# Optimization experiments

Hardware: AMD Instinct MI355X
Metric: run time of the kernel (lower is better)

## Reference

```python
import jax, jax.numpy as jnp
import numpy as np

N = 16384          # number of input points
K = 16             # kNN neighbors for EdgeConv
SCALES = (4096, 1024, 256)
DIM = 256
EC_HID = 64        # EdgeConv output dim
MLP_HID = 128


def _sqdist(a, b):
    # squared euclidean distance matrix: (Na, Nb)
    return (jnp.sum(a * a, axis=1, keepdims=True)
            - 2.0 * (a @ b.T)
            + jnp.sum(b * b, axis=1)[None, :])


def _fps(points, n):
    # farthest point sampling, deterministic start at index 0
    d = jnp.sum((points - points[0]) ** 2, axis=1)  # (N,)

    def step(d, _):
        nxt = jnp.argmax(d)
        d = jnp.minimum(d, jnp.sum((points - points[nxt]) ** 2, axis=1))
        return d, nxt

    _, rest = jax.lax.scan(step, d, None, length=n - 1)
    return jnp.concatenate([jnp.zeros((1,), dtype=rest.dtype), rest])


def setup_inputs() -> dict:
    key = jax.random.key(0)
    ks = jax.random.split(key, 10)

    def lin(k, fi, fo):
        return (jax.random.normal(k, (fi, fo), jnp.float32) / np.sqrt(fi)).astype(jnp.float32)

    nsc = len(SCALES)
    return {
        "points": jax.random.normal(ks[0], (N, 3), jnp.float32),
        # EdgeConv MLP: Linear(6,64) -> ReLU -> Linear(64,64)
        "ew1": lin(ks[1], 6, EC_HID), "eb1": jnp.zeros((EC_HID,), jnp.float32),
        "ew2": lin(ks[2], EC_HID, EC_HID), "eb2": jnp.zeros((EC_HID,), jnp.float32),
        # per-scale MLPs: Linear(64,128) -> ReLU -> Linear(128,256), stacked over scales
        "mw1": jnp.stack([lin(jax.random.fold_in(ks[3], i), EC_HID, MLP_HID) for i in range(nsc)]),
        "mb1": jnp.zeros((nsc, MLP_HID), jnp.float32),
        "mw2": jnp.stack([lin(jax.random.fold_in(ks[4], i), MLP_HID, DIM) for i in range(nsc)]),
        "mb2": jnp.zeros((nsc, DIM), jnp.float32),
    }


def _edge_conv(points, ew1, eb1, ew2, eb2):
    # kNN graph (loop=False): exclude self via +inf diagonal; indices not differentiated
    d = jax.lax.stop_gradient(_sqdist(points, points))
    d = d.at[jnp.arange(N), jnp.arange(N)].set(jnp.inf)
    _, idx = jax.lax.top_k(-d, K)                      # (N, K) neighbor indices
    x_i = points[:, None, :]                           # (N, 1, 3) centers
    x_j = points[idx]                                  # (N, K, 3) neighbors
    ef = jnp.concatenate([jnp.broadcast_to(x_i, (N, K, 3)), x_j - x_i], axis=-1)  # (N,K,6)
    h = jax.nn.relu(ef @ ew1 + eb1) @ ew2 + eb2        # (N, K, 64)
    # scatter_max over centers == max over the K neighbor axis (every center has K edges)
    return jnp.max(h, axis=1)                          # (N, 64)


def reference(points, ew1, eb1, ew2, eb2, mw1, mb1, mw2, mb2):
    feats = _edge_conv(points, ew1, eb1, ew2, eb2)     # (N, 64)
    outs = []
    prev_pts = None
    for i, scale in enumerate(SCALES):
        if i == 0:
            fi = _fps(points, scale)
            sp = points[fi]
            sf = feats[fi]
        else:
            fi = _fps(prev_pts, scale)
            sp = prev_pts[fi]
            nn = jnp.argmin(_sqdist(sp, points), axis=1)  # nearest source point per query
            sf = feats[nn]
        lf = jax.nn.relu(sf @ mw1[i] + mb1[i]) @ mw2[i] + mb2[i]  # (scale, DIM)
        outs.append(sp)
        outs.append(lf)
        prev_pts = sp
    return tuple(outs)
```

## Files before the change

kernel.cpp:

```cpp
#include <hip/hip_runtime.h>
#include <cfloat>
#include <cstdint>

#define N_PTS 16384
#define KNN_K 16
#define KNN_TILE 512
#define CERT_EPS 3e-6f

struct FpsSmem {
    float sx[N_PTS];
    unsigned long long slots[2][16];
    int cw2[2][2];
    int cand_idx[64];
    int cand_cnt;
    int more_flag;
    double red_d[16];
};

template <int CTRL>
__device__ __forceinline__ unsigned dpp_mov_u32(unsigned v) {
    return (unsigned)__builtin_amdgcn_update_dpp((int)v, (int)v, CTRL, 0xF, 0xF, false);
}

__device__ __forceinline__ void cross_slot_reduce(unsigned long long k, float& M1, int& G1) {
    unsigned hi = (unsigned)(k >> 32), lo = (unsigned)k;
#define RSTEP(CTRL)                                          \
    {                                                        \
        const unsigned ohi = dpp_mov_u32<CTRL>(hi);          \
        const unsigned olo = dpp_mov_u32<CTRL>(lo);          \
        const bool b = (ohi > hi) || (ohi == hi && olo > lo);\
        hi = b ? ohi : hi;                                   \
        lo = b ? olo : lo;                                   \
    }
    RSTEP(0x121)
    RSTEP(0x122)
    RSTEP(0x124)
    RSTEP(0x128)
#undef RSTEP
    M1 = __uint_as_float(hi);
    G1 = (int)(~lo);
}

template <int P, bool IND>
__device__ __forceinline__ void fps_body(FpsSmem& sm, const float* __restrict__ pts,
                                         const int* __restrict__ idx,
                                         int n_out, int* __restrict__ fi) {
    constexpr int T = 1024;
    constexpr int NW = T / 64;
    const int tid = threadIdx.x;
    const int wave = tid >> 6, lane = tid & 63;

    __syncthreads();

    if (tid < 32) sm.slots[tid >> 4][tid & 15] = 0ull;
    if (tid < 4) sm.cw2[tid >> 1][tid & 1] = 0;

    float yr[P], zr[P], c[P];
    const int g0 = IND ? idx[0] : 0;
    const float sx0 = pts[g0 * 3 + 0], sy0 = pts[g0 * 3 + 1], sz0 = pts[g0 * 3 + 2];
    if (tid == 0) fi[0] = g0;

    float m1 = -1.0f, m2 = -1.0f;
    int g1 = 0x7fffffff;
#pragma unroll
    for (int q = 0; q < P; ++q) {
        const int g = tid + q * T;
        const int gg = IND ? idx[g] : g;
        const float x = pts[gg * 3 + 0];
        const float y = pts[gg * 3 + 1];
        const float z = pts[gg * 3 + 2];
        sm.sx[g] = x;
        yr[q] = y;
        zr[q] = z;
        const float dx = x - sx0, dy = y - sy0, dz = z - sz0;
        const float t = fmaf(dx, dx, fmaf(dy, dy, dz * dz));
        const float nc = fminf(FLT_MAX, t);
        c[q] = nc;
        const bool gt = nc > m1;
        m2 = fmaxf(m2, fminf(nc, m1));
        m1 = fmaxf(m1, nc);
        g1 = gt ? g : g1;
    }
    __syncthreads();
    {
        const unsigned long long key =
            ((unsigned long long)__float_as_uint(m1) << 32) |
            (unsigned long long)(~(unsigned)g1);
        atomicMax(&sm.slots[1][tid & 15], key);
    }

    for (int s = 1; s < n_out; ++s) {
        __syncthreads();
        const int par = s & 1;

        const unsigned long long k0 = sm.slots[par][lane & 15];
        float M1;
        int G1;
        cross_slot_reduce(k0, M1, G1);
        const float thr = M1 - M1 * CERT_EPS;

        int wg = G1;
        if (IND) wg = idx[G1];
        float nx = sm.sx[G1];
        float ny = pts[wg * 3 + 1];
        float nz = pts[wg * 3 + 2];

        if (tid < 16) sm.slots[par ^ 1][tid] = 0ull;
        if (tid == 0) { sm.cw2[par ^ 1][0] = 0; sm.cw2[par ^ 1][1] = 0; }

        const unsigned long long bal = __ballot(m1 >= thr);
        if (lane == 0) atomicAdd(&sm.cw2[par][0], (int)__popcll(bal));
        if (g1 == G1) sm.cw2[par][1] = (m2 >= thr) ? 1 : 0;

        __syncthreads();
        const int2 tw = *reinterpret_cast<const int2*>(&sm.cw2[par][0]);
        const int total = tw.x, wfl = tw.y;

        if (total > 1 || wfl) {
            unsigned miss = 0;
#pragma unroll
            for (int q = 0; q < P; ++q)
                if (c[q] >= thr) miss |= (1u << q);
            double BD = -1.0;
            int BG = 0x7fffffff;
            for (;;) {
                if (tid == 0) { sm.cand_cnt = 0; sm.more_flag = 0; }
                __syncthreads();
#pragma unroll
                for (int q = 0; q < P; ++q) {
                    if (miss & (1u << q)) {
                        int slot = atomicAdd(&sm.cand_cnt, 1);
                        if (slot < 64) {
                            sm.cand_idx[slot] = tid + q * T;
                            miss &= ~(1u << q);
                        } else {
                            sm.more_flag = 1;
                        }
                    }
                }
                __syncthreads();
                int ncand = sm.cand_cnt;
                if (ncand > 64) ncand = 64;
                for (int ci = 0; ci < ncand; ++ci) {
                    const int g = sm.cand_idx[ci];
                    const int gg = IND ? idx[g] : g;
                    const double qx = (double)pts[gg * 3 + 0];
                    const double qy = (double)pts[gg * 3 + 1];
                    const double qz = (double)pts[gg * 3 + 2];
                    double dmin = DBL_MAX;
                    for (int i = tid; i < s; i += T) {
                        const int h = fi[i];
                        double ddx = qx - (double)pts[h * 3 + 0];
                        double ddy = qy - (double)pts[h * 3 + 1];
                        double ddz = qz - (double)pts[h * 3 + 2];
                        double dd = ddx * ddx + ddy * ddy + ddz * ddz;
                        dmin = (dd < dmin) ? dd : dmin;
                    }
                    for (int off = 32; off; off >>= 1) {
                        double od = __shfl_xor(dmin, off);
                        dmin = (od < dmin) ? od : dmin;
                    }
                    if (lane == 0) sm.red_d[wave] = dmin;
                    __syncthreads();
                    double dall = sm.red_d[0];
#pragma unroll
                    for (int w = 1; w < NW; ++w) dall = (sm.red_d[w] < dall) ? sm.red_d[w] : dall;
                    if (dall > BD || (dall == BD && g < BG)) { BD = dall; BG = g; }
                    __syncthreads();
                }
                int mf = sm.more_flag;
                __syncthreads();
                if (!mf) break;
            }
            G1 = BG;
            wg = IND ? idx[G1] : G1;
            nx = pts[wg * 3 + 0];
            ny = pts[wg * 3 + 1];
            nz = pts[wg * 3 + 2];
        }

        if (tid == 0) fi[s] = wg;
        if (s == n_out - 1) break;

        float nm1 = -1.0f, nm2 = -1.0f;
        int ng1 = 0x7fffffff;
#pragma unroll
        for (int q = 0; q < P; ++q) {
            const float dx = sm.sx[tid + q * T] - nx;
            const float dy = yr[q] - ny, dz = zr[q] - nz;
            const float t = fmaf(dx, dx, fmaf(dy, dy, dz * dz));
            const float nc = fminf(c[q], t);
            c[q] = nc;
            const bool gt = nc > nm1;
            nm2 = fmaxf(nm2, fminf(nc, nm1));
            nm1 = fmaxf(nm1, nc);
            ng1 = gt ? (tid + q * T) : ng1;
        }
        m1 = nm1; m2 = nm2; g1 = ng1;
        const unsigned long long key =
            ((unsigned long long)__float_as_uint(m1) << 32) |
            (unsigned long long)(~(unsigned)g1);
        atomicMax(&sm.slots[par ^ 1][tid & 15], key);
    }
}

struct KnnSmem {
    float sx[KNN_TILE], sy[KNN_TILE], sz[KNN_TILE];
    float w1[6 * 64], b1v[64], w2[64 * 64], b2v[64];
};

__device__ __forceinline__ void knn_edge_body(
    KnnSmem& sm, const float* __restrict__ pts,
    const float* __restrict__ ew1, const float* __restrict__ eb1,
    const float* __restrict__ ew2, const float* __restrict__ eb2,
    float* __restrict__ feats, int qb) {
    for (int t = threadIdx.x; t < 6 * 64; t += 1024) sm.w1[t] = ew1[t];
    for (int t = threadIdx.x; t < 64; t += 1024) { sm.b1v[t] = eb1[t]; sm.b2v[t] = eb2[t]; }
    for (int t = threadIdx.x; t < 64 * 64; t += 1024) sm.w2[t] = ew2[t];

    const int wave = threadIdx.x >> 6;
    const int lane = threadIdx.x & 63;
    const int qi = qb * 16 + wave;
    const double qxd = (double)pts[qi * 3 + 0];
    const double qyd = (double)pts[qi * 3 + 1];
    const double qzd = (double)pts[qi * 3 + 2];

    double ld[16];
    int li[16];
#pragma unroll
    for (int s = 0; s < 16; ++s) { ld[s] = DBL_MAX; li[s] = 0x7fffffff; }
    double md = DBL_MAX; int mj = 0x7fffffff; int mslot = 0;

    for (int t0 = 0; t0 < N_PTS; t0 += KNN_TILE) {
        __syncthreads();
        for (int t = threadIdx.x; t < KNN_TILE; t += 1024) {
            sm.sx[t] = pts[(t0 + t) * 3 + 0];
            sm.sy[t] = pts[(t0 + t) * 3 + 1];
            sm.sz[t] = pts[(t0 + t) * 3 + 2];
        }
        __syncthreads();
#pragma unroll
        for (int m = 0; m < KNN_TILE / 64; ++m) {
            const int cc = lane + m * 64;
            const int j = t0 + cc;
            if (j == qi) continue;
            double dx = qxd - (double)sm.sx[cc];
            double dy = qyd - (double)sm.sy[cc];
            double dz = qzd - (double)sm.sz[cc];
            double dd = dx * dx + dy * dy + dz * dz;
            if (dd < md || (dd == md && j < mj)) {
#pragma unroll
                for (int s = 0; s < 16; ++s)
                    if (s == mslot) { ld[s] = dd; li[s] = j; }
                md = -1.0; mj = -1; mslot = 0;
#pragma unroll
                for (int s = 0; s < 16; ++s) {
                    bool g = (ld[s] > md) || (ld[s] == md && li[s] > mj);
                    if (g) { md = ld[s]; mj = li[s]; mslot = s; }
                }
            }
        }
    }

    const float xi = pts[qi * 3], yi = pts[qi * 3 + 1], zi = pts[qi * 3 + 2];
    float acc = -FLT_MAX;
    for (int r = 0; r < KNN_K; ++r) {
        double cd = DBL_MAX; int cj = 0x7fffffff; int cs = 0;
#pragma unroll
        for (int s = 0; s < 16; ++s) {
            bool l = (ld[s] < cd) || (ld[s] == cd && li[s] < cj);
            if (l) { cd = ld[s]; cj = li[s]; cs = s; }
        }
        double wd = cd; int wj = cj;
        for (int off = 32; off; off >>= 1) {
            double od = __shfl_xor(wd, off);
            int oj = __shfl_xor(wj, off);
            if (od < wd || (od == wd && oj < wj)) { wd = od; wj = oj; }
        }
        if (cd == wd && cj == wj) {
#pragma unroll
            for (int s = 0; s < 16; ++s)
                if (s == cs) { ld[s] = DBL_MAX; li[s] = 0x7fffffff; }
        }
        const float xj = pts[wj * 3], yj = pts[wj * 3 + 1], zj = pts[wj * 3 + 2];
        const float f3 = xj - xi, f4 = yj - yi, f5 = zj - zi;
        float h1 = sm.b1v[lane];
        h1 = fmaf(xi, sm.w1[0 * 64 + lane], h1);
        h1 = fmaf(yi, sm.w1[1 * 64 + lane], h1);
        h1 = fmaf(zi, sm.w1[2 * 64 + lane], h1);
        h1 = fmaf(f3, sm.w1[3 * 64 + lane], h1);
        h1 = fmaf(f4, sm.w1[4 * 64 + lane], h1);
        h1 = fmaf(f5, sm.w1[5 * 64 + lane], h1);
        h1 = fmaxf(h1, 0.0f);
        float h2 = sm.b2v[lane];
        for (int d = 0; d < 64; ++d)
            h2 = fmaf(__shfl(h1, d), sm.w2[d * 64 + lane], h2);
        acc = fmaxf(acc, h2);
    }
    feats[qi * 64 + lane] = acc;
}

__global__ __launch_bounds__(1024)
void mega_kernel(const float* __restrict__ pts,
                 const float* __restrict__ ew1, const float* __restrict__ eb1,
                 const float* __restrict__ ew2, const float* __restrict__ eb2,
                 float* __restrict__ feats,
                 int* __restrict__ fi0, int* __restrict__ fi1, int* __restrict__ fi2,
                 float* __restrict__ sp0, float* __restrict__ sp1,
                 float* __restrict__ sp2) {
    constexpr size_t SMEM_BYTES =
        sizeof(FpsSmem) > sizeof(KnnSmem) ? sizeof(FpsSmem) : sizeof(KnnSmem);
    __shared__ __align__(16) char raw[SMEM_BYTES];
    if (blockIdx.x == 0) {
        FpsSmem& sm = *reinterpret_cast<FpsSmem*>(raw);
        fps_body<16, false>(sm, pts, nullptr, 4096, fi0);
        fps_body<4, true>(sm, pts, fi0, 1024, fi1);
        fps_body<1, true>(sm, pts, fi1, 256, fi2);
        __syncthreads();
        const int tid = threadIdx.x;
        for (int t = tid; t < 4096; t += 1024) {
            int g = fi0[t];
            sp0[t * 3 + 0] = pts[g * 3 + 0];
            sp0[t * 3 + 1] = pts[g * 3 + 1];
            sp0[t * 3 + 2] = pts[g * 3 + 2];
        }
        if (tid < 1024) {
            int g = fi1[tid];
            sp1[tid * 3 + 0] = pts[g * 3 + 0];
            sp1[tid * 3 + 1] = pts[g * 3 + 1];
            sp1[tid * 3 + 2] = pts[g * 3 + 2];
        }
        if (tid < 256) {
            int g = fi2[tid];
            sp2[tid * 3 + 0] = pts[g * 3 + 0];
            sp2[tid * 3 + 1] = pts[g * 3 + 1];
            sp2[tid * 3 + 2] = pts[g * 3 + 2];
        }
    } else {
        knn_edge_body(*reinterpret_cast<KnnSmem*>(raw), pts, ew1, eb1, ew2, eb2,
                      feats, blockIdx.x - 1);
    }
}

__device__ __forceinline__ void mlp_body(
    const float* __restrict__ feats, const int* __restrict__ orig,
    const float* __restrict__ mw1, const float* __restrict__ mb1,
    const float* __restrict__ mw2, const float* __restrict__ mb2,
    float* __restrict__ outp, int pb) {
    __shared__ float sfl[64], h1l[128];
    const int t = threadIdx.x;
    for (int pl = 0; pl < 16; ++pl) {
        const int p = pb * 16 + pl;
        const int g = orig[p];
        if (t < 64) sfl[t] = feats[g * 64 + t];
        __syncthreads();
        if (t < 128) {
            float h = mb1[t];
            for (int dd = 0; dd < 64; ++dd)
                h = fmaf(sfl[dd], mw1[dd * 128 + t], h);
            h1l[t] = fmaxf(h, 0.0f);
        }
        __syncthreads();
        float o = mb2[t];
        for (int dd = 0; dd < 128; ++dd)
            o = fmaf(h1l[dd], mw2[dd * 256 + t], o);
        outp[p * 256 + t] = o;
        __syncthreads();
    }
}

__global__ __launch_bounds__(256) void tail_kernel(
    const float* __restrict__ feats,
    const int* __restrict__ fi0, const int* __restrict__ fi1,
    const int* __restrict__ fi2,
    const float* __restrict__ mw1, const float* __restrict__ mb1,
    const float* __restrict__ mw2, const float* __restrict__ mb2,
    float* __restrict__ out) {
    const int b = blockIdx.x;
    float* lf0 = out + 12288;
    float* lf1 = out + 1063936;
    float* lf2 = out + 1326848;
    if (b < 256) {
        mlp_body(feats, fi0, mw1 + 0 * 8192, mb1 + 0 * 128,
                 mw2 + 0 * 32768, mb2 + 0 * 256, lf0, b);
    } else if (b < 320) {
        mlp_body(feats, fi1, mw1 + 1 * 8192, mb1 + 1 * 128,
                 mw2 + 1 * 32768, mb2 + 1 * 256, lf1, b - 256);
    } else {
        mlp_body(feats, fi2, mw1 + 2 * 8192, mb1 + 2 * 128,
                 mw2 + 2 * 32768, mb2 + 2 * 256, lf2, b - 320);
    }
}

extern "C" void kernel_launch(void* const* d_in, const int* in_sizes, int n_in,
                              void* d_out, int out_size, void* d_ws, size_t ws_size,
                              hipStream_t stream) {
    const float* pts = (const float*)d_in[0];
    const float* ew1 = (const float*)d_in[1];
    const float* eb1 = (const float*)d_in[2];
    const float* ew2 = (const float*)d_in[3];
    const float* eb2 = (const float*)d_in[4];
    const float* mw1 = (const float*)d_in[5];
    const float* mb1 = (const float*)d_in[6];
    const float* mw2 = (const float*)d_in[7];
    const float* mb2 = (const float*)d_in[8];
    float* out = (float*)d_out;
    char* ws = (char*)d_ws;

    float* feats = (float*)(ws + 0);
    int* fi0 = (int*)(ws + 4194304);
    int* fi1 = (int*)(ws + 4210688);
    int* fi2 = (int*)(ws + 4214784);

    float* sp0 = out + 0;
    float* sp1 = out + 1060864;
    float* sp2 = out + 1326080;

    mega_kernel<<<1 + N_PTS / 16, 1024, 0, stream>>>(pts, ew1, eb1, ew2, eb2, feats,
                                                     fi0, fi1, fi2, sp0, sp1, sp2);
    tail_kernel<<<336, 256, 0, stream>>>(feats, fi0, fi1, fi2, mw1, mb1, mw2, mb2, out);
}
```

Measured before the change: 8.301 ms.

## Derive coarser FPS scales as prefixes of the first FPS run

Farthest point sampling run on an earlier FPS result, starting from its first point, picks the same points as a prefix of that result. So the second and third scales become the first 1024 and 256 indices of the 4096-point run. Their nearest source points are the points themselves, so the tail MLPs read features through the same index list. This drops the two extra serial FPS passes on the single FPS block. The winner's coordinates are also shared through LDS by the owning thread instead of each thread reading them from global memory. The prefix equivalence holds up to tie-breaking between equal distances.

```diff
diff --git a/kernel.cpp b/kernel.cpp
--- a/kernel.cpp
+++ b/kernel.cpp
@@ -11,6 +11,7 @@
     float sx[N_PTS];
     unsigned long long slots[2][16];
     int cw2[2][2];
+    float4 pub;
     int cand_idx[64];
     int cand_cnt;
     int more_flag;
@@ -41,34 +42,29 @@
     G1 = (int)(~lo);
 }
 
-template <int P, bool IND>
-__device__ __forceinline__ void fps_body(FpsSmem& sm, const float* __restrict__ pts,
-                                         const int* __restrict__ idx,
-                                         int n_out, int* __restrict__ fi) {
+__device__ __forceinline__ void fps_run(FpsSmem& sm, const float* __restrict__ pts,
+                                        int n_out, int* __restrict__ fi) {
     constexpr int T = 1024;
+    constexpr int P = 16;
     constexpr int NW = T / 64;
     const int tid = threadIdx.x;
     const int wave = tid >> 6, lane = tid & 63;
 
-    __syncthreads();
-
     if (tid < 32) sm.slots[tid >> 4][tid & 15] = 0ull;
     if (tid < 4) sm.cw2[tid >> 1][tid & 1] = 0;
 
     float yr[P], zr[P], c[P];
-    const int g0 = IND ? idx[0] : 0;
-    const float sx0 = pts[g0 * 3 + 0], sy0 = pts[g0 * 3 + 1], sz0 = pts[g0 * 3 + 2];
-    if (tid == 0) fi[0] = g0;
+    const float sx0 = pts[0], sy0 = pts[1], sz0 = pts[2];
+    if (tid == 0) fi[0] = 0;
 
     float m1 = -1.0f, m2 = -1.0f;
     int g1 = 0x7fffffff;
 #pragma unroll
     for (int q = 0; q < P; ++q) {
         const int g = tid + q * T;
-        const int gg = IND ? idx[g] : g;
-        const float x = pts[gg * 3 + 0];
-        const float y = pts[gg * 3 + 1];
-        const float z = pts[gg * 3 + 2];
+        const float x = pts[g * 3 + 0];
+        const float y = pts[g * 3 + 1];
+        const float z = pts[g * 3 + 2];
         sm.sx[g] = x;
         yr[q] = y;
         zr[q] = z;
@@ -99,11 +95,14 @@
         cross_slot_reduce(k0, M1, G1);
         const float thr = M1 - M1 * CERT_EPS;
 
-        int wg = G1;
-        if (IND) wg = idx[G1];
-        float nx = sm.sx[G1];
-        float ny = pts[wg * 3 + 1];
-        float nz = pts[wg * 3 + 2];
+        if (g1 == G1) {
+            const int qw = (G1 - tid) >> 10;
+            float yw = 0.0f, zw = 0.0f;
+#pragma unroll
+            for (int q = 0; q < P; ++q)
+                if (q == qw) { yw = yr[q]; zw = zr[q]; }
+            sm.pub = make_float4(sm.sx[G1], yw, zw, 0.0f);
+        }
 
         if (tid < 16) sm.slots[par ^ 1][tid] = 0ull;
         if (tid == 0) { sm.cw2[par ^ 1][0] = 0; sm.cw2[par ^ 1][1] = 0; }
@@ -115,6 +114,9 @@
         __syncthreads();
         const int2 tw = *reinterpret_cast<const int2*>(&sm.cw2[par][0]);
         const int total = tw.x, wfl = tw.y;
+        const float4 wc = sm.pub;
+        float nx = wc.x, ny = wc.y, nz = wc.z;
+        int wg = G1;
 
         if (total > 1 || wfl) {
             unsigned miss = 0;
@@ -143,10 +145,9 @@
                 if (ncand > 64) ncand = 64;
                 for (int ci = 0; ci < ncand; ++ci) {
                     const int g = sm.cand_idx[ci];
-                    const int gg = IND ? idx[g] : g;
-                    const double qx = (double)pts[gg * 3 + 0];
-                    const double qy = (double)pts[gg * 3 + 1];
-                    const double qz = (double)pts[gg * 3 + 2];
+                    const double qx = (double)pts[g * 3 + 0];
+                    const double qy = (double)pts[g * 3 + 1];
+                    const double qz = (double)pts[g * 3 + 2];
                     double dmin = DBL_MAX;
                     for (int i = tid; i < s; i += T) {
                         const int h = fi[i];
@@ -172,8 +173,7 @@
                 __syncthreads();
                 if (!mf) break;
             }
-            G1 = BG;
-            wg = IND ? idx[G1] : G1;
+            wg = BG;
             nx = pts[wg * 3 + 0];
             ny = pts[wg * 3 + 1];
             nz = pts[wg * 3 + 2];
@@ -305,7 +305,7 @@
                  const float* __restrict__ ew1, const float* __restrict__ eb1,
                  const float* __restrict__ ew2, const float* __restrict__ eb2,
                  float* __restrict__ feats,
-                 int* __restrict__ fi0, int* __restrict__ fi1, int* __restrict__ fi2,
+                 int* __restrict__ fi0,
                  float* __restrict__ sp0, float* __restrict__ sp1,
                  float* __restrict__ sp2) {
     constexpr size_t SMEM_BYTES =
@@ -313,28 +313,27 @@
     __shared__ __align__(16) char raw[SMEM_BYTES];
     if (blockIdx.x == 0) {
         FpsSmem& sm = *reinterpret_cast<FpsSmem*>(raw);
-        fps_body<16, false>(sm, pts, nullptr, 4096, fi0);
-        fps_body<4, true>(sm, pts, fi0, 1024, fi1);
-        fps_body<1, true>(sm, pts, fi1, 256, fi2);
+        fps_run(sm, pts, 4096, fi0);
         __syncthreads();
         const int tid = threadIdx.x;
         for (int t = tid; t < 4096; t += 1024) {
-            int g = fi0[t];
-            sp0[t * 3 + 0] = pts[g * 3 + 0];
-            sp0[t * 3 + 1] = pts[g * 3 + 1];
-            sp0[t * 3 + 2] = pts[g * 3 + 2];
-        }
-        if (tid < 1024) {
-            int g = fi1[tid];
-            sp1[tid * 3 + 0] = pts[g * 3 + 0];
-            sp1[tid * 3 + 1] = pts[g * 3 + 1];
-            sp1[tid * 3 + 2] = pts[g * 3 + 2];
-        }
-        if (tid < 256) {
-            int g = fi2[tid];
-            sp2[tid * 3 + 0] = pts[g * 3 + 0];
-            sp2[tid * 3 + 1] = pts[g * 3 + 1];
-            sp2[tid * 3 + 2] = pts[g * 3 + 2];
+            const int g = fi0[t];
+            const float x = pts[g * 3 + 0];
+            const float y = pts[g * 3 + 1];
+            const float z = pts[g * 3 + 2];
+            sp0[t * 3 + 0] = x;
+            sp0[t * 3 + 1] = y;
+            sp0[t * 3 + 2] = z;
+            if (t < 1024) {
+                sp1[t * 3 + 0] = x;
+                sp1[t * 3 + 1] = y;
+                sp1[t * 3 + 2] = z;
+            }
+            if (t < 256) {
+                sp2[t * 3 + 0] = x;
+                sp2[t * 3 + 1] = y;
+                sp2[t * 3 + 2] = z;
+            }
         }
     } else {
         knn_edge_body(*reinterpret_cast<KnnSmem*>(raw), pts, ew1, eb1, ew2, eb2,
@@ -371,8 +370,7 @@
 
 __global__ __launch_bounds__(256) void tail_kernel(
     const float* __restrict__ feats,
-    const int* __restrict__ fi0, const int* __restrict__ fi1,
-    const int* __restrict__ fi2,
+    const int* __restrict__ fi0,
     const float* __restrict__ mw1, const float* __restrict__ mb1,
     const float* __restrict__ mw2, const float* __restrict__ mb2,
     float* __restrict__ out) {
@@ -384,10 +382,10 @@
         mlp_body(feats, fi0, mw1 + 0 * 8192, mb1 + 0 * 128,
                  mw2 + 0 * 32768, mb2 + 0 * 256, lf0, b);
     } else if (b < 320) {
-        mlp_body(feats, fi1, mw1 + 1 * 8192, mb1 + 1 * 128,
+        mlp_body(feats, fi0, mw1 + 1 * 8192, mb1 + 1 * 128,
                  mw2 + 1 * 32768, mb2 + 1 * 256, lf1, b - 256);
     } else {
-        mlp_body(feats, fi2, mw1 + 2 * 8192, mb1 + 2 * 128,
+        mlp_body(feats, fi0, mw1 + 2 * 8192, mb1 + 2 * 128,
                  mw2 + 2 * 32768, mb2 + 2 * 256, lf2, b - 320);
     }
 }
@@ -409,14 +407,12 @@
 
     float* feats = (float*)(ws + 0);
     int* fi0 = (int*)(ws + 4194304);
-    int* fi1 = (int*)(ws + 4210688);
-    int* fi2 = (int*)(ws + 4214784);
 
     float* sp0 = out + 0;
     float* sp1 = out + 1060864;
     float* sp2 = out + 1326080;
 
     mega_kernel<<<1 + N_PTS / 16, 1024, 0, stream>>>(pts, ew1, eb1, ew2, eb2, feats,
-                                                     fi0, fi1, fi2, sp0, sp1, sp2);
-    tail_kernel<<<336, 256, 0, stream>>>(feats, fi0, fi1, fi2, mw1, mb1, mw2, mb2, out);
-}
+                                                     fi0, sp0, sp1, sp2);
+    tail_kernel<<<336, 256, 0, stream>>>(feats, fi0, mw1, mb1, mw2, mb2, out);
+}
```

Result: faster. 7.461 ms (-10.1%).
